# Performance work log

Measured on AMD Instinct MI355X. Metric: run time of the kernel, lower is better.

The kernel has to match this reference:

```python
import jax, jax.numpy as jnp
import numpy as np

THRESHOLD1 = 1.0
THRESHOLD2 = 1.0


def _conv(x, w, stride, pad):
    return jax.lax.conv_general_dilated(
        x, w, window_strides=(stride, stride),
        padding=((pad, pad), (pad, pad)),
        dimension_numbers=('NCHW', 'OIHW', 'NCHW'))


def _percentiles_1_to_99(t):
    # Faithful to torch: k = 1 + round(0.01*q*(n-1)); kthvalue = k-th smallest.
    # One sort + static gather replaces 99 kthvalue calls.
    flat = jnp.sort(t.reshape(-1))
    n = flat.shape[0]  # static under jit
    ks = np.array([1 + round(0.01 * q * (n - 1)) for q in range(1, 100)], dtype=np.int64)
    return flat[ks - 1]  # [99]


def setup_inputs() -> dict:
    key = jax.random.key(0)
    k1, k2, k3, k4 = jax.random.split(key, 4)
    x = jax.random.normal(k1, (64, 128, 56, 56), jnp.float32)
    # Kaiming-ish scaled conv weights
    w1 = jax.random.normal(k2, (256, 128, 3, 3), jnp.float32) * (2.0 / (128 * 9)) ** 0.5
    w2 = jax.random.normal(k3, (256, 256, 3, 3), jnp.float32) * (2.0 / (256 * 9)) ** 0.5
    w_id = jax.random.normal(k4, (256, 128, 1, 1), jnp.float32) * (2.0 / 128) ** 0.5
    return {"x": x, "w1": w1, "w2": w2, "w_id": w_id}


def reference(x, w1, w2, w_id):
    out1 = _conv(x, w1, 2, 1)                 # conv1: [64,256,28,28]
    a = _percentiles_1_to_99(out1)            # percentiles of UNclamped conv1 output
    out = jnp.clip(out1, 0.0, THRESHOLD1)     # out[out>t1]=t1; out[out<0]=0
    # dropout(p=0.0 / eval) is identity
    out = _conv(out, w2, 1, 1)                # conv2
    out = out + _conv(x, w_id, 2, 0)          # residual via 1x1 stride-2 downsample
    b = _percentiles_1_to_99(out)             # percentiles before second clamp
    out = jnp.clip(out, 0.0, THRESHOLD2)
    return out, a, b
```

## Files before the change

kernel.cpp:

```cpp
#include <hip/hip_runtime.h>

typedef unsigned short ushort_t;
typedef unsigned int uint_t;

using short8 = __attribute__((ext_vector_type(8))) short;
using f32x4  = __attribute__((ext_vector_type(4))) float;

#define N_BATCH   64
#define C_MID     256
#define H_OUT     28
#define W_OUT     28
#define SPATIAL   (H_OUT*W_OUT)
#define OUT_ELEMS (N_BATCH*C_MID*SPATIAL)

#define NBINS 2048
#define BIN_LO (-16.0f)
#define BIN_INV 64.0f
#define BIN_W  0.015625f

#define XT_ROW   (57*128)
#define XT_IMG   (57*57*128)
#define O1_ROW   (30*256)
#define O1_IMG   (30*30*256)

#define WAITVM(n) asm volatile("s_waitcnt vmcnt(" #n ")" ::: "memory")
#define BARRIER() asm volatile("s_barrier" ::: "memory")

__device__ __forceinline__ ushort_t f2bf(float f) {
    uint_t u = __float_as_uint(f);
    u += 0x7FFFu + ((u >> 16) & 1u);
    return (ushort_t)(u >> 16);
}

__device__ __forceinline__ void gll16(const ushort_t* g, void* l) {
    __builtin_amdgcn_global_load_lds(
        (const __attribute__((address_space(1))) unsigned int*)g,
        (__attribute__((address_space(3))) unsigned int*)l, 16, 0, 0);
}

__global__ __launch_bounds__(256) void zwtrans(
    uint_t* __restrict__ xT32, uint_t* __restrict__ o1T32,
    const float* __restrict__ w1, const float* __restrict__ w2,
    const float* __restrict__ wid, ushort_t* __restrict__ wT1,
    ushort_t* __restrict__ wT2, uint_t* __restrict__ hfA,
    uint_t* __restrict__ hfB)
{
    const int bxx = blockIdx.x, y = blockIdx.y, tid = threadIdx.x;
    if (bxx < 87) {
        int i = bxx * 256 + tid;
        int n = y;
        if (i >= 22080) return;
        if (i < 7232) {
            uint_t* base = xT32 + (size_t)n * (XT_IMG / 2);
            if (i < 3648) base[i] = 0;
            else { int j = i - 3648; int r = (j >> 6) + 1;
                   base[r * (XT_ROW / 2) + (j & 63)] = 0; }
        } else {
            int k = i - 7232;
            uint_t* base = o1T32 + (size_t)n * (O1_IMG / 2);
            if (k < 3840) base[k] = 0;
            else if (k < 7680) base[29 * (O1_ROW / 2) + (k - 3840)] = 0;
            else if (k < 11264) { int j = k - 7680; int r = (j >> 7) + 1;
                   base[r * (O1_ROW / 2) + (j & 127)] = 0; }
            else { int j = k - 11264; int r = (j >> 7) + 1;
                   base[r * (O1_ROW / 2) + 29 * 128 + (j & 127)] = 0; }
        }
    } else {
        int idx = ((bxx - 87) * 64 + y) * 256 + tid;
        if (idx < 2048)      hfA[idx] = 0;
        else if (idx < 4096) hfB[idx - 2048] = 0;
        if (idx < 256 * 1152) {
            int co = idx / 1152, k = idx % 1152;
            int g = k >> 7, ci = k & 127;
            wT1[idx] = f2bf(w1[(co * 128 + ci) * 9 + g]);
        }
        if (idx < 256 * 2432) {
            int co = idx / 2432, k = idx % 2432;
            float v;
            if (k < 2304) { int g = k >> 8, ci = k & 255; v = w2[(co * 256 + ci) * 9 + g]; }
            else          { v = wid[co * 128 + (k - 2304)]; }
            wT2[idx] = f2bf(v);
        }
    }
}

__global__ __launch_bounds__(256) void xtrans(
    const float* __restrict__ x, ushort_t* __restrict__ xT)
{
    __shared__ ushort_t t[224 * 130];
    const int tid = threadIdx.x;
    const int g = blockIdx.x, n = blockIdx.y;
    const float* xs = x + ((size_t)n * 128) * 3136 + g * 4 * 56;

    #pragma unroll
    for (int it = 0; it < 28; ++it) {
        int f = it * 256 + tid;
        int ci = f / 56, r4 = f % 56;
        float4 v = *(const float4*)(xs + ci * 3136 + r4 * 4);
        t[(r4 * 4 + 0) * 130 + ci] = f2bf(v.x);
        t[(r4 * 4 + 1) * 130 + ci] = f2bf(v.y);
        t[(r4 * 4 + 2) * 130 + ci] = f2bf(v.z);
        t[(r4 * 4 + 3) * 130 + ci] = f2bf(v.w);
    }
    __syncthreads();
    ushort_t* xo = xT + (size_t)n * XT_IMG + (g * 4 + 1) * XT_ROW + 128;
    for (int it = 0; it < 56; ++it) {
        int f = it * 256 + tid;
        int pos = f >> 6, c2 = f & 63;
        int r = pos / 56, iw = pos % 56;
        uint_t v = *(const uint_t*)&t[pos * 130 + c2 * 2];
        *(uint_t*)(xo + r * XT_ROW + iw * 128 + c2 * 2) = v;
    }
}

__global__ __launch_bounds__(256, 2) void conv1_mfma(
    const ushort_t* __restrict__ xT, const ushort_t* __restrict__ wT1,
    ushort_t* __restrict__ o1T, uint_t* __restrict__ hf)
{
    const int bx = blockIdx.x;
    const int tid = threadIdx.x;
    const int wv = tid >> 6, lane = tid & 63;
    const int ln = lane & 15, quad = lane >> 4;
    const int n = bx / 7, rg = bx % 7, r0 = rg * 4;

    __shared__ short8 Ald[2 * 1024];
    __shared__ short8 Bp[2304];

    f32x4 acc[4][7];
    #pragma unroll
    for (int a = 0; a < 4; ++a)
        #pragma unroll
        for (int b = 0; b < 7; ++b) acc[a][b] = (f32x4){0.f, 0.f, 0.f, 0.f};

    int drb[7], cl0[7];
    #pragma unroll
    for (int b = 0; b < 7; ++b) {
        int p = b * 16 + ln;
        drb[b] = 2 * (p / 28);
        cl0[b] = p % 28;
    }

    uint_t poff[9];
    #pragma unroll
    for (int i = 0; i < 9; ++i) {
        int slot = (i * 4 + wv) * 64 + lane;
        int s2 = min(slot, 2051);
        int k8 = s2 / 513;
        int rem = s2 - k8 * 513;
        int dr = rem / 57, j = rem - dr * 57;
        int col = (j < 29) ? (2 * j) : (2 * (j - 29) + 1);
        poff[i] = (uint_t)((2 * r0 + dr) * XT_ROW + col * 128 + k8 * 8);
    }
    const uint_t aoff = (uint_t)((wv * 64 + lane) * 1152);

    const ushort_t* xTimg = xT + (size_t)n * XT_IMG;

    auto stageA = [&](int tap, int c, int buf) {
        #pragma unroll
        for (int jj = 0; jj < 4; ++jj)
            gll16(wT1 + aoff + jj * 8 + tap * 128 + c * 32,
                  (char*)Ald + buf * 16384 + (jj * 256 + wv * 64) * 16);
    };

    for (int c = 0; c < 4; ++c) {
        BARRIER();
        #pragma unroll
        for (int i = 0; i < 9; ++i)
            gll16(xTimg + poff[i] + c * 32, (char*)Bp + ((i * 4 + wv) * 64) * 16);
        if (c == 0) stageA(0, 0, 0);
        WAITVM(0);
        BARRIER();

        #pragma unroll
        for (int t = 0; t < 9; ++t) {
            const int st = c * 9 + t;
            const int buf = st & 1;
            if (t < 8)      stageA(t + 1, c, buf ^ 1);
            else if (c < 3) stageA(0, c + 1, buf ^ 1);
            if (c == 3 && t == 8) { WAITVM(0); } else { WAITVM(4); }
            const int kh = t / 3, kw = t - kh * 3;
            short8 af[4], bf[7];
            #pragma unroll
            for (int a = 0; a < 4; ++a)
                af[a] = Ald[buf * 1024 + quad * 256 + wv * 64 + a * 16 + ln];
            #pragma unroll
            for (int b = 0; b < 7; ++b) {
                int dr = drb[b] + kh;
                int j = (kw == 1) ? (29 + cl0[b]) : (cl0[b] + (kw >> 1));
                bf[b] = Bp[quad * 513 + dr * 57 + j];
            }
            __builtin_amdgcn_s_setprio(1);
            #pragma unroll
            for (int a = 0; a < 4; ++a)
                #pragma unroll
                for (int b = 0; b < 7; ++b)
                    acc[a][b] = __builtin_amdgcn_mfma_f32_16x16x32_bf16(
                        af[a], bf[b], acc[a][b], 0, 0, 0);
            __builtin_amdgcn_s_setprio(0);
        }
    }

    __syncthreads();
    uint_t* hist = (uint_t*)Ald;
    for (int i = tid; i < NBINS; i += 256) hist[i] = 0;
    __syncthreads();

    ushort_t* oimg = o1T + (size_t)n * O1_IMG;
    #pragma unroll
    for (int a = 0; a < 4; ++a) {
        int co = wv * 64 + a * 16 + quad * 4;
        #pragma unroll
        for (int b = 0; b < 7; ++b) {
            int p = b * 16 + ln;
            int h = r0 + p / 28, w = p % 28;
            ushort_t pk[4];
            #pragma unroll
            for (int r = 0; r < 4; ++r) {
                float v = acc[a][b][r];
                int bin = (int)((v - BIN_LO) * BIN_INV);
                bin = min(max(bin, 0), NBINS - 1);
                atomicAdd(&hist[bin], 1u);
                pk[r] = f2bf(fminf(fmaxf(v, 0.f), 1.f));
            }
            uint2 u; u.x = (uint_t)pk[0] | ((uint_t)pk[1] << 16);
            u.y = (uint_t)pk[2] | ((uint_t)pk[3] << 16);
            *(uint2*)(oimg + ((h + 1) * 30 + (w + 1)) * 256 + co) = u;
        }
    }

    __syncthreads();
    for (int i = tid; i < NBINS; i += 256) {
        uint_t v = hist[i];
        if (v) atomicAdd(&hf[i], v);
    }
}

__global__ __launch_bounds__(256, 2) void conv2_mfma(
    const ushort_t* __restrict__ o1T, const ushort_t* __restrict__ xT,
    const ushort_t* __restrict__ wT2, float* __restrict__ fout,
    uint_t* __restrict__ hf)
{
    const int bx = blockIdx.x;
    const int by = blockIdx.y;
    const int tid = threadIdx.x;
    const int wv = tid >> 6, lane = tid & 63;
    const int ln = lane & 15, quad = lane >> 4;
    const int n = bx >> 2, rg = bx & 3, r0 = rg * 8;
    const int coh = wv & 1;
    const int pt  = wv >> 1;

    __shared__ short8 Ad[3 * 512];
    __shared__ short8 Bp[2 * 1280];

    f32x4 acc[4][7];
    #pragma unroll
    for (int a = 0; a < 4; ++a)
        #pragma unroll
        for (int b = 0; b < 7; ++b) acc[a][b] = (f32x4){0.f, 0.f, 0.f, 0.f};

    int prb[7], cl0[7], hlog[7];
    #pragma unroll
    for (int b = 0; b < 7; ++b) {
        int p = b * 16 + ln;
        int h = r0 + pt * 4 + p / 28;
        hlog[b] = h;
        prb[b] = (min(h, 27) - r0) * 32;
        cl0[b] = p % 28;
    }

    uint_t po[5];
    #pragma unroll
    for (int jj = 0; jj < 5; ++jj) {
        int f = (wv * 5 + jj) * 64 + lane;
        int ci8 = f / 320, rem = f % 320;
        int dr = rem >> 5, cl = rem & 31;
        po[jj] = (uint_t)(min(r0 + dr, 29) * O1_ROW + cl * 256 + ci8 * 8);
    }
    uint_t io[4];
    #pragma unroll
    for (int jj = 0; jj < 4; ++jj) {
        int i2 = min(wv * 4 + jj, 13);
        int slot = i2 * 64 + lane;
        int ci8 = slot / 224, pos = slot % 224;
        int h = min(r0 + pos / 28, 27), w = pos % 28;
        io[jj] = (uint_t)(((2 * h + 1) * 57 + (2 * w + 1)) * 128 + ci8 * 8);
    }

    const ushort_t* o1img = o1T + (size_t)n * O1_IMG;
    const ushort_t* xTimg = xT + (size_t)n * XT_IMG;
    const ushort_t* Ab0 = wT2 + (size_t)(by * 128 + lane) * 2432 + wv * 8;
    const ushort_t* Ab1 = Ab0 + (size_t)64 * 2432;

    auto stageA = [&](int k0, int buf) {
        gll16(Ab0 + k0, (char*)Ad + buf * 8192 + wv * 2048);
        gll16(Ab1 + k0, (char*)Ad + buf * 8192 + wv * 2048 + 1024);
    };
    auto stageB = [&](int hb, int coff) {
        #pragma unroll
        for (int jj = 0; jj < 5; ++jj)
            gll16(o1img + po[jj] + coff, (char*)Bp + hb * 20480 + (wv * 5 + jj) * 1024);
    };
    auto stageI = [&](int ib, int idh) {
        #pragma unroll
        for (int jj = 0; jj < 4; ++jj) {
            int i2 = min(wv * 4 + jj, 13);
            gll16(xTimg + io[jj] + idh * 32, (char*)Bp + ib * 20480 + i2 * 1024);
        }
    };

    stageB(0, 0);
    stageA(0, 0);

    for (int h = 0; h < 8; ++h) {
        #pragma unroll
        for (int t = 0; t < 9; ++t) {
            if (t < 8)      stageA((t + 1) * 256 + h * 32, (t + 1) % 3);
            else if (h < 7) stageA((h + 1) * 32, 0);
            else            stageA(2304, 0);
            if (t == 1) {
                if (h < 7) { stageB((h + 1) & 1, (h + 1) * 32); WAITVM(7); }
                else       { stageI(0, 0);                      WAITVM(6); }
            } else {
                WAITVM(2);
            }
            BARRIER();
            const int abuf = t % 3;
            const int kh = t / 3, kw = t - kh * 3;
            short8 af[4], bf[7];
            #pragma unroll
            for (int a = 0; a < 4; ++a)
                af[a] = Ad[abuf * 512 + quad * 128 + coh * 64 + a * 16 + ln];
            #pragma unroll
            for (int b = 0; b < 7; ++b)
                bf[b] = Bp[(h & 1) * 1280 + quad * 320 + prb[b] + kh * 32 + cl0[b] + kw];
            __builtin_amdgcn_s_setprio(1);
            #pragma unroll
            for (int a = 0; a < 4; ++a)
                #pragma unroll
                for (int b = 0; b < 7; ++b)
                    acc[a][b] = __builtin_amdgcn_mfma_f32_16x16x32_bf16(
                        af[a], bf[b], acc[a][b], 0, 0, 0);
            __builtin_amdgcn_s_setprio(0);
        }
    }

    #pragma unroll
    for (int idh = 0; idh < 4; ++idh) {
        if (idh < 3) { stageA(2304 + (idh + 1) * 32, (idh + 1) % 3); WAITVM(2); }
        else         { WAITVM(0); }
        BARRIER();
        if (idh < 3) stageI((idh + 1) & 1, idh + 1);
        short8 af[4], bf[7];
        #pragma unroll
        for (int a = 0; a < 4; ++a)
            af[a] = Ad[(idh % 3) * 512 + quad * 128 + coh * 64 + a * 16 + ln];
        #pragma unroll
        for (int b = 0; b < 7; ++b)
            bf[b] = Bp[(idh & 1) * 1280 + quad * 224 + pt * 112 + b * 16 + ln];
        __builtin_amdgcn_s_setprio(1);
        #pragma unroll
        for (int a = 0; a < 4; ++a)
            #pragma unroll
            for (int b = 0; b < 7; ++b)
                acc[a][b] = __builtin_amdgcn_mfma_f32_16x16x32_bf16(
                    af[a], bf[b], acc[a][b], 0, 0, 0);
        __builtin_amdgcn_s_setprio(0);
    }

    __syncthreads();
    uint_t* hist = (uint_t*)Ad;
    for (int i = tid; i < NBINS; i += 256) hist[i] = 0;
    __syncthreads();

    #pragma unroll
    for (int a = 0; a < 4; ++a) {
        int co = by * 128 + coh * 64 + a * 16 + quad * 4;
        #pragma unroll
        for (int b = 0; b < 7; ++b) {
            if (hlog[b] <= 27) {
                #pragma unroll
                for (int r = 0; r < 4; ++r) {
                    float v = acc[a][b][r];
                    int bin = (int)((v - BIN_LO) * BIN_INV);
                    bin = min(max(bin, 0), NBINS - 1);
                    atomicAdd(&hist[bin], 1u);
                    fout[((size_t)(n * 256 + co + r)) * SPATIAL +
                         hlog[b] * 28 + cl0[b]] = fminf(fmaxf(v, 0.f), 1.f);
                }
            }
        }
    }

    __syncthreads();
    for (int i = tid; i < NBINS; i += 256) {
        uint_t v = hist[i];
        if (v) atomicAdd(&hf[i], v);
    }
}

__global__ __launch_bounds__(1024) void select_k(
    const uint_t* __restrict__ hfA, const uint_t* __restrict__ hfB,
    float* __restrict__ outp)
{
    const uint_t* hf = blockIdx.x ? hfB : hfA;
    float* op = outp + blockIdx.x * 99;
    __shared__ uint_t cs[1024];
    int t = threadIdx.x;
    uint_t s = hf[2 * t] + hf[2 * t + 1];
    cs[t] = s;
    __syncthreads();
    for (int d = 1; d < 1024; d <<= 1) {
        uint_t v = (t >= d) ? cs[t - d] : 0;
        __syncthreads();
        cs[t] += v;
        __syncthreads();
    }
    if (t >= 1 && t <= 99) {
        long long k = 1 + (long long)llrint(0.01 * (double)t * (double)(OUT_ELEMS - 1));
        int lo = 0, hi = 1023;
        while (lo < hi) { int mid = (lo + hi) >> 1; if ((long long)cs[mid] < k) lo = mid + 1; else hi = mid; }
        long long cum = (lo == 0) ? 0 : (long long)cs[lo - 1];
        int b = lo * 2;
        while (cum + (long long)hf[b] < k) { cum += hf[b]; ++b; }
        op[t - 1] = BIN_LO + ((float)b + 0.5f) * BIN_W;
    }
}

extern "C" void kernel_launch(void* const* d_in, const int* in_sizes, int n_in,
                              void* d_out, int out_size, void* d_ws, size_t ws_size,
                              hipStream_t stream)
{
    const float* x   = (const float*)d_in[0];
    const float* w1  = (const float*)d_in[1];
    const float* w2  = (const float*)d_in[2];
    const float* wid = (const float*)d_in[3];
    float* out = (float*)d_out;

    char* ws = (char*)d_ws;
    ushort_t* xT  = (ushort_t*)ws;
    ushort_t* o1T = (ushort_t*)(ws + 53235712);
    ushort_t* wT1 = (ushort_t*)(ws + 82731008);
    ushort_t* wT2 = (ushort_t*)(ws + 83320832);
    uint_t*   hfA = (uint_t*)  (ws + 88498176);
    uint_t*   hfB = (uint_t*)  (ws + 88506368);

    zwtrans<<<dim3(125, 64), 256, 0, stream>>>((uint_t*)xT, (uint_t*)o1T,
                                               w1, w2, wid, wT1, wT2, hfA, hfB);
    xtrans<<<dim3(14, 64), 256, 0, stream>>>(x, xT);

    conv1_mfma<<<448, 256, 0, stream>>>(xT, wT1, o1T, hfA);
    conv2_mfma<<<dim3(256, 2), 256, 0, stream>>>(o1T, xT, wT2, out, hfB);

    select_k<<<2, 1024, 0, stream>>>(hfA, hfB, out + OUT_ELEMS);
}
```

Measured before the change: 340.3 us.

## Pair conv2 K-steps per barrier with a 4-slot weight ring buffer

Restructures the conv2 main loop so each barrier covers two K-steps (two 3x3 taps) instead of one. The weight staging buffer grows from 3 to 4 slots, and weights are prefetched two steps ahead. The aim is to halve the number of barriers and vmcnt waits and give more MFMA work between synchronisations. In exchange it uses more LDS, which can cut occupancy, and it waits with vmcnt(0) rather than allowing partial outstanding loads.

```diff
diff --git a/kernel.cpp b/kernel.cpp
--- a/kernel.cpp
+++ b/kernel.cpp
@@ -249,7 +249,7 @@
     const int coh = wv & 1;
     const int pt  = wv >> 1;
 
-    __shared__ short8 Ad[3 * 512];
+    __shared__ short8 Ad[4 * 512];
     __shared__ short8 Bp[2 * 1280];
 
     f32x4 acc[4][7];
@@ -291,9 +291,9 @@
     const ushort_t* Ab0 = wT2 + (size_t)(by * 128 + lane) * 2432 + wv * 8;
     const ushort_t* Ab1 = Ab0 + (size_t)64 * 2432;
 
-    auto stageA = [&](int k0, int buf) {
-        gll16(Ab0 + k0, (char*)Ad + buf * 8192 + wv * 2048);
-        gll16(Ab1 + k0, (char*)Ad + buf * 8192 + wv * 2048 + 1024);
+    auto stageA = [&](int k0, int slot) {
+        gll16(Ab0 + k0, (char*)Ad + slot * 8192 + wv * 2048);
+        gll16(Ab1 + k0, (char*)Ad + slot * 8192 + wv * 2048 + 1024);
     };
     auto stageB = [&](int hb, int coff) {
         #pragma unroll
@@ -308,52 +308,75 @@
         }
     };
 
+#define STEP_MFMA(SL, HD, T) do {                                             \
+    const int kh_ = (T) / 3, kw_ = (T) % 3;                                   \
+    short8 af_[4], bf_[7];                                                    \
+    _Pragma("unroll")                                                         \
+    for (int a_ = 0; a_ < 4; ++a_)                                            \
+        af_[a_] = Ad[(SL) * 512 + quad * 128 + coh * 64 + a_ * 16 + ln];      \
+    _Pragma("unroll")                                                         \
+    for (int b_ = 0; b_ < 7; ++b_)                                            \
+        bf_[b_] = Bp[(HD) * 1280 + quad * 320 + prb[b_] +                     \
+                     kh_ * 32 + cl0[b_] + kw_];                               \
+    __builtin_amdgcn_s_setprio(1);                                            \
+    _Pragma("unroll")                                                         \
+    for (int a_ = 0; a_ < 4; ++a_)                                            \
+        _Pragma("unroll")                                                     \
+        for (int b_ = 0; b_ < 7; ++b_)                                        \
+            acc[a_][b_] = __builtin_amdgcn_mfma_f32_16x16x32_bf16(            \
+                af_[a_], bf_[b_], acc[a_][b_], 0, 0, 0);                      \
+    __builtin_amdgcn_s_setprio(0);                                            \
+} while (0)
+
+#define PAIR(Q) do {                                                          \
+    const int c0 = 2 * (Q), c1 = c0 + 1;                                      \
+    const int t0_ = c0 % 9, t1_ = c1 % 9;                                     \
+    const int hd0 = c0 / 9, hd1 = c1 / 9;                                     \
+    WAITVM(0);                                                                \
+    BARRIER();                                                                \
+    {                                       \
+        const int u0 = c0 + 2, u1 = c0 + 3;                                   \
+        int k0_, k1_;                                                         \
+        if (u0 < 18) k0_ = (u0 % 9) * 256 + (hh * 2 + u0 / 9) * 32;           \
+        else k0_ = lastsup ? 2304                                             \
+                           : ((u0 - 18) % 9) * 256 + (hh * 2 + 2) * 32;       \
+        if (u1 < 18) k1_ = (u1 % 9) * 256 + (hh * 2 + u1 / 9) * 32;           \
+        else k1_ = lastsup ? (2304 + (u1 - 18) * 32)                          \
+                           : ((u1 - 18) % 9) * 256 + (hh * 2 + 2) * 32;       \
+        stageA(k0_, (hh * 18 + u0) & 3);                                      \
+        stageA(k1_, (hh * 18 + u1) & 3);                                      \
+    }                                                                         \
+    if ((Q) == 0) {                                  \
+        stageB(1, (hh * 2 + 1) * 32);                                         \
+    } else if ((Q) == 5) {                           \
+        if (!lastsup) stageB(0, (hh * 2 + 2) * 32);                           \
+        else          stageI(0, 0);                                           \
+    }                                                                         \
+    STEP_MFMA((hh * 18 + c0) & 3, hd0, t0_);                                  \
+    STEP_MFMA((hh * 18 + c1) & 3, hd1, t1_);                                  \
+} while (0)
+
+    stageA(0, 0);
+    stageA(256, 1);
     stageB(0, 0);
-    stageA(0, 0);
-
-    for (int h = 0; h < 8; ++h) {
-        #pragma unroll
-        for (int t = 0; t < 9; ++t) {
-            if (t < 8)      stageA((t + 1) * 256 + h * 32, (t + 1) % 3);
-            else if (h < 7) stageA((h + 1) * 32, 0);
-            else            stageA(2304, 0);
-            if (t == 1) {
-                if (h < 7) { stageB((h + 1) & 1, (h + 1) * 32); WAITVM(7); }
-                else       { stageI(0, 0);                      WAITVM(6); }
-            } else {
-                WAITVM(2);
-            }
-            BARRIER();
-            const int abuf = t % 3;
-            const int kh = t / 3, kw = t - kh * 3;
-            short8 af[4], bf[7];
-            #pragma unroll
-            for (int a = 0; a < 4; ++a)
-                af[a] = Ad[abuf * 512 + quad * 128 + coh * 64 + a * 16 + ln];
-            #pragma unroll
-            for (int b = 0; b < 7; ++b)
-                bf[b] = Bp[(h & 1) * 1280 + quad * 320 + prb[b] + kh * 32 + cl0[b] + kw];
-            __builtin_amdgcn_s_setprio(1);
-            #pragma unroll
-            for (int a = 0; a < 4; ++a)
-                #pragma unroll
-                for (int b = 0; b < 7; ++b)
-                    acc[a][b] = __builtin_amdgcn_mfma_f32_16x16x32_bf16(
-                        af[a], bf[b], acc[a][b], 0, 0, 0);
-            __builtin_amdgcn_s_setprio(0);
-        }
-    }
+
+    for (int hh = 0; hh < 4; ++hh) {
+        const bool lastsup = (hh == 3);
+        PAIR(0); PAIR(1); PAIR(2); PAIR(3); PAIR(4);
+        PAIR(5); PAIR(6); PAIR(7); PAIR(8);
+    }
+#undef PAIR
 
     #pragma unroll
     for (int idh = 0; idh < 4; ++idh) {
-        if (idh < 3) { stageA(2304 + (idh + 1) * 32, (idh + 1) % 3); WAITVM(2); }
-        else         { WAITVM(0); }
+        WAITVM(0);
         BARRIER();
+        if (idh < 2) stageA(2304 + (idh + 2) * 32, idh + 2);
         if (idh < 3) stageI((idh + 1) & 1, idh + 1);
         short8 af[4], bf[7];
         #pragma unroll
         for (int a = 0; a < 4; ++a)
-            af[a] = Ad[(idh % 3) * 512 + quad * 128 + coh * 64 + a * 16 + ln];
+            af[a] = Ad[idh * 512 + quad * 128 + coh * 64 + a * 16 + ln];
         #pragma unroll
         for (int b = 0; b < 7; ++b)
             bf[b] = Bp[(idh & 1) * 1280 + quad * 224 + pt * 112 + b * 16 + ln];
@@ -366,6 +389,7 @@
                     af[a], bf[b], acc[a][b], 0, 0, 0);
         __builtin_amdgcn_s_setprio(0);
     }
+#undef STEP_MFMA
 
     __syncthreads();
     uint_t* hist = (uint_t*)Ad;
```

New measurement: 340.0 us. No clear change (-0.1%).
